# Kernel tuning notes

Measured on AMD Instinct MI355X. Metric: run time of the kernel, lower is better.

The kernel has to match this reference:

```python
import jax, jax.numpy as jnp
import numpy as np
import math


def setup_inputs() -> dict:
    key = jax.random.key(0)
    k_fm, k_x, k_y, k_w, k_h = jax.random.split(key, 5)
    C, H, W = 512, 256, 256
    N = 4096
    patch_num = 4
    pe = 2  # sqrt(patch_num)
    feature_map = jax.random.normal(k_fm, (C, H, W), dtype=jnp.float32)
    # Boxes fully inside the map with per-patch extent >= 2 so every sub-box is valid.
    min_wh = 2.0 * pe + 1.0
    x0 = jax.random.uniform(k_x, (N,), minval=0.0, maxval=W / 2 - 1.0)
    y0 = jax.random.uniform(k_y, (N,), minval=0.0, maxval=H / 2 - 1.0)
    w = jax.random.uniform(k_w, (N,), minval=min_wh, maxval=W / 2 - 2.0)
    h = jax.random.uniform(k_h, (N,), minval=min_wh, maxval=H / 2 - 2.0)
    roi_batch = jnp.stack([x0, y0, x0 + w, y0 + h], axis=1).astype(jnp.float32)
    return {"feature_map": feature_map, "roi_batch": roi_batch, "patch_num": patch_num}


def _box_indices(roi_batch, patch_num, W):
    """Rounded, clamped per-patch sub-box corners; shapes (P, N), flattened patch-major."""
    pe = int(math.isqrt(patch_num))
    xmin, ymin, xmax, ymax = (roi_batch[:, k] for k in range(4))
    i = jnp.arange(patch_num)
    ix = (i % pe).astype(roi_batch.dtype)[:, None]
    iy = (i // pe).astype(roi_batch.dtype)[:, None]
    ws = ((xmax - xmin) / pe)[None, :]
    hs = ((ymax - ymin) / pe)[None, :]
    ax = xmin[None, :] + ix * ws  # (P, N)
    ay = ymin[None, :] + iy * hs
    clampi = lambda v: jnp.clip(jnp.round(v), 0, W - 1).astype(jnp.int32)
    x0, x1 = clampi(ax), clampi(ax + ws)
    y0, y1 = clampi(ay), clampi(ay + hs)
    flat = lambda a: a.reshape(-1)  # loop order: patch outer, roi inner
    return flat(x0), flat(x1), flat(y0), flat(y1)


def reference(feature_map, roi_batch, patch_num):
    C, H, W = feature_map.shape
    x0, x1, y0, y1 = _box_indices(roi_batch, patch_num, W)
    cw = x1 - x0
    ch = y1 - y0
    mask = (cw >= 1) & (ch >= 1)  # (P*N,)
    # Integral image with zero row/col padding: S[:, y, x] = sum of fm[:, :y, :x]
    S = jnp.pad(jnp.cumsum(jnp.cumsum(feature_map, axis=1), axis=2),
                ((0, 0), (1, 0), (1, 0)))
    # Region sums via 4-corner gather: (C, B)
    sums = S[:, y1, x1] - S[:, y0, x1] - S[:, y1, x0] + S[:, y0, x0]
    area = jnp.maximum(cw * ch, 1).astype(feature_map.dtype)
    pooled = (sums / area).T  # (B, C) region means == adaptive_avg_pool2d(.,(1,1))
    pooled = pooled * mask.astype(feature_map.dtype)[:, None]
    return pooled[:, :, None, None], mask.astype(jnp.int32)
```

## Files before the change

kernel.cpp:

```cpp
#include <hip/hip_runtime.h>


#define CHN 512
#define WD  256
#define SP  257
#define YC  8
#define NK  32
#define CB  32
#define GCH 256
#define SLICE_OFF 16908544UL

#define SIDX(cb, y, x)   ((((size_t)(cb) * SP + (y)) * SP + (x)) * CB)
#define OPIDX(cb, kk, x) ((((size_t)(cb) * 33 + (kk)) * SP + (x)) * CB)

typedef float f32x4v __attribute__((ext_vector_type(4)));

__device__ __forceinline__ float4 ntld4(const float* p) {
    f32x4v u = __builtin_nontemporal_load((const f32x4v*)p);
    return make_float4(u.x, u.y, u.z, u.w);
}

#define BAR() do { asm volatile("s_waitcnt lgkmcnt(0)" ::: "memory"); \
                   __builtin_amdgcn_s_barrier(); \
                   asm volatile("" ::: "memory"); } while (0)

__global__ __launch_bounds__(512, 4) void fusedScanK(const float* __restrict__ fm,
                                                     float* __restrict__ S) {
    __shared__ float tile[2][CB][260];
    const int t = threadIdx.x, lane = t & 63, w = t >> 6;
    const int cb = blockIdx.x;
    const int c0 = cb * CB;
    const int k  = blockIdx.y;
    const int y0 = k * YC;

    const int cg = t & 7;
    const int x8 = t >> 3;
    const float4 z4 = make_float4(0.f, 0.f, 0.f, 0.f);

    if (k == 0) {
        #pragma unroll
        for (int it = 0; it < 4; ++it) {
            const int lin = it * 512 + t;
            const int cgg = lin & 7, x = lin >> 3;
            *(float4*)(S + SIDX(cb, 0, x) + 4 * cgg) = z4;
        }
    }

    float4 cur[4], nxt[4];
    #pragma unroll
    for (int j = 0; j < 4; ++j)
        cur[j] = ntld4(fm + ((size_t)(c0 + w * 4 + j) << 16)
                          + (size_t)y0 * 256 + 4 * lane);

    float4 acc[4];
    #pragma unroll
    for (int m = 0; m < 4; ++m) acc[m] = z4;

    const int wcol = (4 * lane) ^ (4 * w);
    const int rxor = 4 * cg;

    for (int y = 0; y < YC; ++y) {
        const int buf = y & 1;
        if (y < YC - 1) {
            #pragma unroll
            for (int j = 0; j < 4; ++j)
                nxt[j] = ntld4(fm + ((size_t)(c0 + w * 4 + j) << 16)
                                  + (size_t)(y0 + y + 1) * 256 + 4 * lane);
        }
        #pragma unroll
        for (int j = 0; j < 4; ++j) {
            const float4 v = cur[j];
            const float local = ((v.x + v.y) + v.z) + v.w;
            float s = local;
            #pragma unroll
            for (int d = 1; d < 64; d <<= 1) {
                float u = __shfl_up(s, d, 64);
                if (lane >= d) s += u;
            }
            const float e = s - local;
            float4 p;
            p.x = e   + v.x;
            p.y = p.x + v.y;
            p.z = p.y + v.z;
            p.w = p.z + v.w;
            *(float4*)&tile[buf][w * 4 + j][wcol] = p;
        }
        BAR();
        const size_t rowb = SIDX(cb, y0 + y + 1, 0);
        #pragma unroll
        for (int m = 0; m < 4; ++m) {
            const int x = x8 + 64 * m;
            const int xs = x ^ rxor;
            float4 a = acc[m];
            a.x += tile[buf][4 * cg + 0][xs];
            a.y += tile[buf][4 * cg + 1][xs];
            a.z += tile[buf][4 * cg + 2][xs];
            a.w += tile[buf][4 * cg + 3][xs];
            acc[m] = a;
            *(float4*)(S + rowb + (size_t)(x + 1) * CB + 4 * cg) = a;
        }
        if (t < 8)
            *(float4*)(S + rowb + 4 * t) = z4;
        #pragma unroll
        for (int j = 0; j < 4; ++j) cur[j] = nxt[j];
    }
}

__global__ __launch_bounds__(256) void offsetK(const float* __restrict__ S,
                                               float* __restrict__ OP) {
    const int gid = blockIdx.x * 256 + threadIdx.x;
    const int cc = gid & 31;
    const int xr = gid >> 5;
    const int x  = xr % SP;
    const int cb = xr / SP;
    OP[OPIDX(cb, 0, x) + cc] = 0.0f;
    OP[OPIDX(cb, 1, x) + cc] = 0.0f;
    double run = 0.0;
    #pragma unroll
    for (int j = 0; j < NK - 1; ++j) {
        run += (double)S[SIDX(cb, YC * (j + 1), x) + cc];
        OP[OPIDX(cb, j + 2, x) + cc] = (float)run;
    }
}

__global__ __launch_bounds__(256) void gatherK(const float* __restrict__ S,
                                              const float* __restrict__ OP,
                                              const float* __restrict__ roi,
                                              float* __restrict__ out,
                                              float* __restrict__ maskOut,
                                              int N, int writeMask) {
    const int t = threadIdx.x;
    const int tl = t & 127;
    const int n = blockIdx.x * 2 + (t >> 7);
    const float xmin = roi[4 * n + 0];
    const float ymin = roi[4 * n + 1];
    const float xmax = roi[4 * n + 2];
    const float ymax = roi[4 * n + 3];

    const float wsv = __fdiv_rn(__fsub_rn(xmax, xmin), 2.0f);
    const float hsv = __fdiv_rn(__fsub_rn(ymax, ymin), 2.0f);
    const float ax1 = __fadd_rn(xmin, wsv);
    const float ay1 = __fadd_rn(ymin, hsv);
    const float lim = (float)(WD - 1);

    int rx[3], ry[3];
    rx[0] = (int)fminf(fmaxf(rintf(xmin), 0.0f), lim);
    rx[1] = (int)fminf(fmaxf(rintf(ax1), 0.0f), lim);
    rx[2] = (int)fminf(fmaxf(rintf(__fadd_rn(ax1, wsv)), 0.0f), lim);
    ry[0] = (int)fminf(fmaxf(rintf(ymin), 0.0f), lim);
    ry[1] = (int)fminf(fmaxf(rintf(ay1), 0.0f), lim);
    ry[2] = (int)fminf(fmaxf(rintf(__fadd_rn(ay1, hsv)), 0.0f), lim);

    const int cbb = tl >> 4;
    const int cc  = (tl & 15) * 2;
    float2 g[3][3];
    #pragma unroll
    for (int j = 0; j < 3; ++j) {
        const int kk = (ry[j] + YC - 1) >> 3;
        #pragma unroll
        for (int i = 0; i < 3; ++i) {
            const float2 l = *(const float2*)(S  + SIDX(cbb, ry[j], rx[i]) + cc);
            const float2 o = *(const float2*)(OP + OPIDX(cbb, kk, rx[i]) + cc);
            g[j][i] = make_float2(l.x + o.x, l.y + o.y);
        }
    }

    float m[4];
    #pragma unroll
    for (int p = 0; p < 4; ++p) {
        const int ix = p & 1, iy = p >> 1;
        const int cw = rx[ix + 1] - rx[ix];
        const int ch = ry[iy + 1] - ry[iy];
        const int maskv = (cw >= 1 && ch >= 1) ? 1 : 0;
        int areai = cw * ch; if (areai < 1) areai = 1;
        const float areaf = (float)areai;
        const float maskf = (float)maskv;
        m[p] = maskf;

        const float2 s11 = g[iy + 1][ix + 1];
        const float2 s01 = g[iy][ix + 1];
        const float2 s10 = g[iy + 1][ix];
        const float2 s00 = g[iy][ix];
        float2 o;
        o.x = __fdiv_rn(((s11.x - s01.x) - s10.x) + s00.x, areaf) * maskf;
        o.y = __fdiv_rn(((s11.y - s01.y) - s10.y) + s00.y, areaf) * maskf;
        *(float2*)(out + ((size_t)p * N + n) * CHN + 2 * tl) = o;
    }
    if (writeMask && tl < 4) maskOut[(size_t)tl * N + n] = m[tl];
}

extern "C" void kernel_launch(void* const* d_in, const int* in_sizes, int n_in,
                              void* d_out, int out_size, void* d_ws, size_t ws_size,
                              hipStream_t stream) {
    const float* fm  = (const float*)d_in[0];
    const float* roi = (const float*)d_in[1];

    const int N = in_sizes[1] / 4;
    const int B = 4 * N;

    float* S  = (float*)d_ws;
    float* OP = (float*)d_ws + SLICE_OFF;
    float* out     = (float*)d_out;
    float* maskOut = out + (size_t)B * CHN;

    for (int g = 0; g < 2; ++g) {
        const float* fm_g = fm + ((size_t)(g * GCH) << 16);
        dim3 gF(GCH / CB, NK);
        fusedScanK<<<gF, 512, 0, stream>>>(fm_g, S);

        offsetK<<<(8 * SP * CB) / 256, 256, 0, stream>>>(S, OP);

        gatherK<<<N / 2, 256, 0, stream>>>(S, OP, roi,
                                           out + (size_t)g * GCH, maskOut,
                                           N, g == 0 ? 1 : 0);
    }
}
```

Before: 246.6 us.

## Double-buffer workspace and co-schedule scan, offset and gather across channel halves

Splits the two channel-half passes into separate S/OP workspace buffers so the second half's scan can run in the same launch as the first half's offset pass, and the second half's offset pass in the same launch as the first half's gather. This cuts the launch count from six to four and lets independent stages overlap on the GPU instead of serialising. It also drops the unused final S row (256 rows instead of 257) and widens gather blocks to 512 threads covering four ROIs. The cost is a larger workspace and mixed-role blocks whose different register and LDS needs may lower occupancy.

```diff
diff --git a/kernel.cpp b/kernel.cpp
--- a/kernel.cpp
+++ b/kernel.cpp
@@ -4,14 +4,20 @@
 #define CHN 512
 #define WD  256
 #define SP  257
+#define YS  256
 #define YC  8
 #define NK  32
 #define CB  32
 #define GCH 256
-#define SLICE_OFF 16908544UL
-
-#define SIDX(cb, y, x)   ((((size_t)(cb) * SP + (y)) * SP + (x)) * CB)
+
+#define SIDX(cb, y, x)   ((((size_t)(cb) * YS + (y)) * SP + (x)) * CB)
 #define OPIDX(cb, kk, x) ((((size_t)(cb) * 33 + (kk)) * SP + (x)) * CB)
+
+#define S_SZ  ((size_t)8 * YS * SP * CB)
+#define OP_SZ ((size_t)8 * 33 * SP * CB)
+
+#define OFF_UNITS 129
+#define GATH_UNITS 1024
 
 typedef float f32x4v __attribute__((ext_vector_type(4)));
 
@@ -24,13 +30,13 @@
                    __builtin_amdgcn_s_barrier(); \
                    asm volatile("" ::: "memory"); } while (0)
 
-__global__ __launch_bounds__(512, 4) void fusedScanK(const float* __restrict__ fm,
-                                                     float* __restrict__ S) {
-    __shared__ float tile[2][CB][260];
+__device__ __forceinline__ void scanBody(const float* __restrict__ fm,
+                                         float* __restrict__ S,
+                                         int bid, float tile[2][CB][260]) {
     const int t = threadIdx.x, lane = t & 63, w = t >> 6;
-    const int cb = blockIdx.x;
+    const int cb = bid & 7;
     const int c0 = cb * CB;
-    const int k  = blockIdx.y;
+    const int k  = bid >> 3;
     const int y0 = k * YC;
 
     const int cg = t & 7;
@@ -86,7 +92,8 @@
             *(float4*)&tile[buf][w * 4 + j][wcol] = p;
         }
         BAR();
-        const size_t rowb = SIDX(cb, y0 + y + 1, 0);
+        const int rowY = y0 + y + 1;
+        const size_t rowb = SIDX(cb, rowY, 0);
         #pragma unroll
         for (int m = 0; m < 4; ++m) {
             const int x = x8 + 64 * m;
@@ -97,18 +104,20 @@
             a.z += tile[buf][4 * cg + 2][xs];
             a.w += tile[buf][4 * cg + 3][xs];
             acc[m] = a;
-            *(float4*)(S + rowb + (size_t)(x + 1) * CB + 4 * cg) = a;
-        }
-        if (t < 8)
+            if (rowY < YS)
+                *(float4*)(S + rowb + (size_t)(x + 1) * CB + 4 * cg) = a;
+        }
+        if (rowY < YS && t < 8)
             *(float4*)(S + rowb + 4 * t) = z4;
         #pragma unroll
         for (int j = 0; j < 4; ++j) cur[j] = nxt[j];
     }
 }
 
-__global__ __launch_bounds__(256) void offsetK(const float* __restrict__ S,
-                                               float* __restrict__ OP) {
-    const int gid = blockIdx.x * 256 + threadIdx.x;
+__device__ __forceinline__ void offsetBody(const float* __restrict__ S,
+                                           float* __restrict__ OP, int u) {
+    const int gid = u * 512 + threadIdx.x;
+    if (gid >= 8 * SP * CB) return;
     const int cc = gid & 31;
     const int xr = gid >> 5;
     const int x  = xr % SP;
@@ -123,15 +132,15 @@
     }
 }
 
-__global__ __launch_bounds__(256) void gatherK(const float* __restrict__ S,
-                                              const float* __restrict__ OP,
-                                              const float* __restrict__ roi,
-                                              float* __restrict__ out,
-                                              float* __restrict__ maskOut,
-                                              int N, int writeMask) {
+__device__ __forceinline__ void gatherBody(const float* __restrict__ S,
+                                           const float* __restrict__ OP,
+                                           const float* __restrict__ roi,
+                                           float* __restrict__ out,
+                                           float* __restrict__ maskOut,
+                                           int N, int writeMask, int u) {
     const int t = threadIdx.x;
     const int tl = t & 127;
-    const int n = blockIdx.x * 2 + (t >> 7);
+    const int n = u * 4 + (t >> 7);
     const float xmin = roi[4 * n + 0];
     const float ymin = roi[4 * n + 1];
     const float xmax = roi[4 * n + 2];
@@ -189,6 +198,44 @@
     if (writeMask && tl < 4) maskOut[(size_t)tl * N + n] = m[tl];
 }
 
+__global__ __launch_bounds__(512, 4) void scanK(const float* __restrict__ fm,
+                                                float* __restrict__ S) {
+    __shared__ float tile[2][CB][260];
+    scanBody(fm, S, blockIdx.x, tile);
+}
+
+__global__ __launch_bounds__(512, 4) void scanOffK(const float* __restrict__ fm,
+                                                   float* __restrict__ Sdst,
+                                                   const float* __restrict__ Ssrc,
+                                                   float* __restrict__ OPsrc) {
+    __shared__ float tile[2][CB][260];
+    const int bid = blockIdx.x;
+    if (bid < 256) scanBody(fm, Sdst, bid, tile);
+    else           offsetBody(Ssrc, OPsrc, bid - 256);
+}
+
+__global__ __launch_bounds__(512) void gathOffK(const float* __restrict__ S,
+                                                const float* __restrict__ OP,
+                                                const float* __restrict__ roi,
+                                                float* __restrict__ out,
+                                                float* __restrict__ maskOut,
+                                                int N, int writeMask,
+                                                const float* __restrict__ Sn,
+                                                float* __restrict__ OPn) {
+    const int bid = blockIdx.x;
+    if (bid < OFF_UNITS) offsetBody(Sn, OPn, bid);
+    else gatherBody(S, OP, roi, out, maskOut, N, writeMask, bid - OFF_UNITS);
+}
+
+__global__ __launch_bounds__(512) void gathK(const float* __restrict__ S,
+                                             const float* __restrict__ OP,
+                                             const float* __restrict__ roi,
+                                             float* __restrict__ out,
+                                             float* __restrict__ maskOut,
+                                             int N, int writeMask) {
+    gatherBody(S, OP, roi, out, maskOut, N, writeMask, blockIdx.x);
+}
+
 extern "C" void kernel_launch(void* const* d_in, const int* in_sizes, int n_in,
                               void* d_out, int out_size, void* d_ws, size_t ws_size,
                               hipStream_t stream) {
@@ -198,20 +245,21 @@
     const int N = in_sizes[1] / 4;
     const int B = 4 * N;
 
-    float* S  = (float*)d_ws;
-    float* OP = (float*)d_ws + SLICE_OFF;
+    float* S_A  = (float*)d_ws;
+    float* OP_A = S_A + S_SZ;
+    float* S_B  = OP_A + OP_SZ;
+    float* OP_B = S_B + S_SZ;
     float* out     = (float*)d_out;
     float* maskOut = out + (size_t)B * CHN;
 
-    for (int g = 0; g < 2; ++g) {
-        const float* fm_g = fm + ((size_t)(g * GCH) << 16);
-        dim3 gF(GCH / CB, NK);
-        fusedScanK<<<gF, 512, 0, stream>>>(fm_g, S);
-
-        offsetK<<<(8 * SP * CB) / 256, 256, 0, stream>>>(S, OP);
-
-        gatherK<<<N / 2, 256, 0, stream>>>(S, OP, roi,
-                                           out + (size_t)g * GCH, maskOut,
-                                           N, g == 0 ? 1 : 0);
-    }
-}
+    const float* fm0 = fm;
+    const float* fm1 = fm + ((size_t)GCH << 16);
+
+    scanK<<<256, 512, 0, stream>>>(fm0, S_A);
+    scanOffK<<<256 + OFF_UNITS, 512, 0, stream>>>(fm1, S_B, S_A, OP_A);
+    gathOffK<<<OFF_UNITS + GATH_UNITS, 512, 0, stream>>>(S_A, OP_A, roi,
+                                                         out, maskOut, N, 1,
+                                                         S_B, OP_B);
+    gathK<<<GATH_UNITS, 512, 0, stream>>>(S_B, OP_B, roi,
+                                          out + GCH, maskOut, N, 0);
+}
```

Measured after the change: 254.8 us. 3.3% more time.

## Merge both channel-half scans into single launches and widen gather loads to float4

Applied to the files above, without the earlier changes.

Both 256-channel groups now get their own workspace buffers, so the scan and offset passes for both halves each run in one launch with twice the blocks. This removes the serial dependency between halves and gives each launch more parallelism. The S row dimension shrinks to 256 by skipping the unused last row. The gather kernel now handles four ROIs per block with float4 loads and stores instead of float2, which cuts per-thread instruction count. In exchange, workspace use roughly doubles.

```diff
diff --git a/kernel.cpp b/kernel.cpp
--- a/kernel.cpp
+++ b/kernel.cpp
@@ -4,14 +4,19 @@
 #define CHN 512
 #define WD  256
 #define SP  257
+#define YS  256
 #define YC  8
 #define NK  32
 #define CB  32
 #define GCH 256
-#define SLICE_OFF 16908544UL
-
-#define SIDX(cb, y, x)   ((((size_t)(cb) * SP + (y)) * SP + (x)) * CB)
+
+#define SIDX(cb, y, x)   ((((size_t)(cb) * YS + (y)) * SP + (x)) * CB)
 #define OPIDX(cb, kk, x) ((((size_t)(cb) * 33 + (kk)) * SP + (x)) * CB)
+
+#define S_SZ  ((size_t)8 * YS * SP * CB)
+#define OP_SZ ((size_t)8 * 33 * SP * CB)
+
+#define OFF_UNITS 129
 
 typedef float f32x4v __attribute__((ext_vector_type(4)));
 
@@ -24,13 +29,13 @@
                    __builtin_amdgcn_s_barrier(); \
                    asm volatile("" ::: "memory"); } while (0)
 
-__global__ __launch_bounds__(512, 4) void fusedScanK(const float* __restrict__ fm,
-                                                     float* __restrict__ S) {
-    __shared__ float tile[2][CB][260];
+__device__ __forceinline__ void scanBody(const float* __restrict__ fm,
+                                         float* __restrict__ S,
+                                         int bid, float tile[2][CB][260]) {
     const int t = threadIdx.x, lane = t & 63, w = t >> 6;
-    const int cb = blockIdx.x;
+    const int cb = bid & 7;
     const int c0 = cb * CB;
-    const int k  = blockIdx.y;
+    const int k  = bid >> 3;
     const int y0 = k * YC;
 
     const int cg = t & 7;
@@ -86,7 +91,8 @@
             *(float4*)&tile[buf][w * 4 + j][wcol] = p;
         }
         BAR();
-        const size_t rowb = SIDX(cb, y0 + y + 1, 0);
+        const int rowY = y0 + y + 1;
+        const size_t rowb = SIDX(cb, rowY, 0);
         #pragma unroll
         for (int m = 0; m < 4; ++m) {
             const int x = x8 + 64 * m;
@@ -97,18 +103,37 @@
             a.z += tile[buf][4 * cg + 2][xs];
             a.w += tile[buf][4 * cg + 3][xs];
             acc[m] = a;
-            *(float4*)(S + rowb + (size_t)(x + 1) * CB + 4 * cg) = a;
-        }
-        if (t < 8)
+            if (rowY < YS)
+                *(float4*)(S + rowb + (size_t)(x + 1) * CB + 4 * cg) = a;
+        }
+        if (rowY < YS && t < 8)
             *(float4*)(S + rowb + 4 * t) = z4;
         #pragma unroll
         for (int j = 0; j < 4; ++j) cur[j] = nxt[j];
     }
 }
 
-__global__ __launch_bounds__(256) void offsetK(const float* __restrict__ S,
-                                               float* __restrict__ OP) {
-    const int gid = blockIdx.x * 256 + threadIdx.x;
+__global__ __launch_bounds__(512, 4) void scanK(const float* __restrict__ fm,
+                                                float* __restrict__ S_A,
+                                                float* __restrict__ S_B) {
+    __shared__ float tile[2][CB][260];
+    const int bid = blockIdx.x;
+    const int g = bid >> 8;
+    const float* fm_g = fm + ((size_t)(g * GCH) << 16);
+    float* Sg = g ? S_B : S_A;
+    scanBody(fm_g, Sg, bid & 255, tile);
+}
+
+__global__ __launch_bounds__(512) void offK(const float* __restrict__ S_A,
+                                            float* __restrict__ OP_A,
+                                            const float* __restrict__ S_B,
+                                            float* __restrict__ OP_B) {
+    int u = blockIdx.x;
+    const float* S = (u < OFF_UNITS) ? S_A : S_B;
+    float* OP      = (u < OFF_UNITS) ? OP_A : OP_B;
+    if (u >= OFF_UNITS) u -= OFF_UNITS;
+    const int gid = u * 512 + threadIdx.x;
+    if (gid >= 8 * SP * CB) return;
     const int cc = gid & 31;
     const int xr = gid >> 5;
     const int x  = xr % SP;
@@ -123,15 +148,15 @@
     }
 }
 
-__global__ __launch_bounds__(256) void gatherK(const float* __restrict__ S,
-                                              const float* __restrict__ OP,
-                                              const float* __restrict__ roi,
-                                              float* __restrict__ out,
-                                              float* __restrict__ maskOut,
-                                              int N, int writeMask) {
+__global__ __launch_bounds__(256) void gathK(const float* __restrict__ S,
+                                             const float* __restrict__ OP,
+                                             const float* __restrict__ roi,
+                                             float* __restrict__ out,
+                                             float* __restrict__ maskOut,
+                                             int N, int writeMask) {
     const int t = threadIdx.x;
-    const int tl = t & 127;
-    const int n = blockIdx.x * 2 + (t >> 7);
+    const int tl = t & 63;
+    const int n = blockIdx.x * 4 + (t >> 6);
     const float xmin = roi[4 * n + 0];
     const float ymin = roi[4 * n + 1];
     const float xmax = roi[4 * n + 2];
@@ -151,17 +176,17 @@
     ry[1] = (int)fminf(fmaxf(rintf(ay1), 0.0f), lim);
     ry[2] = (int)fminf(fmaxf(rintf(__fadd_rn(ay1, hsv)), 0.0f), lim);
 
-    const int cbb = tl >> 4;
-    const int cc  = (tl & 15) * 2;
-    float2 g[3][3];
+    const int cbb = tl >> 3;
+    const int cc  = (tl & 7) * 4;
+    float4 g[3][3];
     #pragma unroll
     for (int j = 0; j < 3; ++j) {
         const int kk = (ry[j] + YC - 1) >> 3;
         #pragma unroll
         for (int i = 0; i < 3; ++i) {
-            const float2 l = *(const float2*)(S  + SIDX(cbb, ry[j], rx[i]) + cc);
-            const float2 o = *(const float2*)(OP + OPIDX(cbb, kk, rx[i]) + cc);
-            g[j][i] = make_float2(l.x + o.x, l.y + o.y);
+            const float4 l = *(const float4*)(S  + SIDX(cbb, ry[j], rx[i]) + cc);
+            const float4 o = *(const float4*)(OP + OPIDX(cbb, kk, rx[i]) + cc);
+            g[j][i] = make_float4(l.x + o.x, l.y + o.y, l.z + o.z, l.w + o.w);
         }
     }
 
@@ -177,14 +202,16 @@
         const float maskf = (float)maskv;
         m[p] = maskf;
 
-        const float2 s11 = g[iy + 1][ix + 1];
-        const float2 s01 = g[iy][ix + 1];
-        const float2 s10 = g[iy + 1][ix];
-        const float2 s00 = g[iy][ix];
-        float2 o;
+        const float4 s11 = g[iy + 1][ix + 1];
+        const float4 s01 = g[iy][ix + 1];
+        const float4 s10 = g[iy + 1][ix];
+        const float4 s00 = g[iy][ix];
+        float4 o;
         o.x = __fdiv_rn(((s11.x - s01.x) - s10.x) + s00.x, areaf) * maskf;
         o.y = __fdiv_rn(((s11.y - s01.y) - s10.y) + s00.y, areaf) * maskf;
-        *(float2*)(out + ((size_t)p * N + n) * CHN + 2 * tl) = o;
+        o.z = __fdiv_rn(((s11.z - s01.z) - s10.z) + s00.z, areaf) * maskf;
+        o.w = __fdiv_rn(((s11.w - s01.w) - s10.w) + s00.w, areaf) * maskf;
+        *(float4*)(out + ((size_t)p * N + n) * CHN + 4 * tl) = o;
     }
     if (writeMask && tl < 4) maskOut[(size_t)tl * N + n] = m[tl];
 }
@@ -198,20 +225,15 @@
     const int N = in_sizes[1] / 4;
     const int B = 4 * N;
 
-    float* S  = (float*)d_ws;
-    float* OP = (float*)d_ws + SLICE_OFF;
+    float* S_A  = (float*)d_ws;
+    float* OP_A = S_A + S_SZ;
+    float* S_B  = OP_A + OP_SZ;
+    float* OP_B = S_B + S_SZ;
     float* out     = (float*)d_out;
     float* maskOut = out + (size_t)B * CHN;
 
-    for (int g = 0; g < 2; ++g) {
-        const float* fm_g = fm + ((size_t)(g * GCH) << 16);
-        dim3 gF(GCH / CB, NK);
-        fusedScanK<<<gF, 512, 0, stream>>>(fm_g, S);
-
-        offsetK<<<(8 * SP * CB) / 256, 256, 0, stream>>>(S, OP);
-
-        gatherK<<<N / 2, 256, 0, stream>>>(S, OP, roi,
-                                           out + (size_t)g * GCH, maskOut,
-                                           N, g == 0 ? 1 : 0);
-    }
-}
+    scanK<<<512, 512, 0, stream>>>(fm, S_A, S_B);
+    offK<<<2 * OFF_UNITS, 512, 0, stream>>>(S_A, OP_A, S_B, OP_B);
+    gathK<<<N / 4, 256, 0, stream>>>(S_A, OP_A, roi, out, maskOut, N, 1);
+    gathK<<<N / 4, 256, 0, stream>>>(S_B, OP_B, roi, out + GCH, maskOut, N, 0);
+}
```

Result: slower. 252.6 us (+2.4%).
